# Optimization experiments

Measured on AMD Instinct MI355X. Metric: run time of the kernel, lower is better.

Reference implementation:

```python
import jax, jax.numpy as jnp
import numpy as np

N_EMBD = 384
N_HEADS = 6
HEAD_SIZE = N_EMBD // N_HEADS  # 64
D_FF = 4 * N_EMBD
EPS = 1e-5


def layernorm(x, g, b):
    mu = jnp.mean(x, axis=-1, keepdims=True)
    var = jnp.var(x, axis=-1, keepdims=True)
    return (x - mu) * jax.lax.rsqrt(var + EPS) * g + b


def setup_inputs() -> dict:
    key = jax.random.key(0)
    ks = jax.random.split(key, 12)
    B, T, C, H, HS = 64, 256, N_EMBD, N_HEADS, HEAD_SIZE
    s = 0.02
    return {
        "x": jax.random.normal(ks[0], (B, T, C), jnp.float32),
        "Wq": jax.random.normal(ks[1], (H, C, HS), jnp.float32) * s,
        "Wk": jax.random.normal(ks[2], (H, C, HS), jnp.float32) * s,
        "Wv": jax.random.normal(ks[3], (H, C, HS), jnp.float32) * s,
        "Wo": jax.random.normal(ks[4], (C, C), jnp.float32) * s,
        "bo": jnp.zeros((C,), jnp.float32),
        "W1": jax.random.normal(ks[5], (C, D_FF), jnp.float32) * s,
        "b1": jnp.zeros((D_FF,), jnp.float32),
        "W2": jax.random.normal(ks[6], (D_FF, C), jnp.float32) * s,
        "b2": jnp.zeros((C,), jnp.float32),
        "g1": jnp.ones((C,), jnp.float32),
        "beta1": jnp.zeros((C,), jnp.float32),
        "g2": jnp.ones((C,), jnp.float32),
        "beta2": jnp.zeros((C,), jnp.float32),
    }


def reference(x, Wq, Wk, Wv, Wo, bo, W1, b1, W2, b2, g1, beta1, g2, beta2):
    B, T, C = x.shape
    # --- attention branch (dropout = identity in eval) ---
    h = layernorm(x, g1, beta1)
    q = jnp.einsum('btc,hck->bhtk', h, Wq)
    k = jnp.einsum('btc,hck->bhtk', h, Wk)
    v = jnp.einsum('btc,hck->bhtk', h, Wv)
    scale = HEAD_SIZE ** -0.5
    wei = jnp.einsum('bhtk,bhsk->bhts', q, k) * scale  # [B,H,T,T]
    causal = jnp.tril(jnp.ones((T, T), bool))
    wei = jnp.where(causal, wei, -jnp.inf)
    wei = jax.nn.softmax(wei, axis=-1)
    attn = jnp.einsum('bhts,bhsk->bthk', wei, v).reshape(B, T, C)
    x = x + attn @ Wo + bo
    # --- MLP branch ---
    h2 = layernorm(x, g2, beta2)
    ff = jax.nn.relu(h2 @ W1 + b1) @ W2 + b2
    return x + ff
```

## Files before the change

### kernel.cpp

```cpp
#include <hip/hip_runtime.h>

#define B 64
#define T 256
#define C 384
#define H 6
#define HS 64
#define DFF 1536
#define BT (B*T)

typedef __attribute__((ext_vector_type(8))) short short8;
typedef __attribute__((ext_vector_type(4))) float float4v;
typedef __attribute__((ext_vector_type(4))) unsigned short ushort4v;

static __device__ __forceinline__ unsigned short f2bf(float f) {
  unsigned int u = __float_as_uint(f);
  unsigned int r = (u + 0x7fffu + ((u >> 16) & 1u)) >> 16;
  return (unsigned short)r;
}

typedef __attribute__((address_space(1))) const unsigned int ga_u32;
typedef __attribute__((address_space(3))) unsigned int ls_u32;
static __device__ __forceinline__ void gld16(const void* g, void* l) {
  __builtin_amdgcn_global_load_lds((ga_u32*)g, (ls_u32*)l, 16, 0, 0);
}

__global__ __launch_bounds__(256) void prep_w(
    const float* __restrict__ Wq, const float* __restrict__ Wk, const float* __restrict__ Wv,
    const float* __restrict__ Wo, const float* __restrict__ W1, const float* __restrict__ W2,
    unsigned short* __restrict__ wqkv, unsigned short* __restrict__ wo,
    unsigned short* __restrict__ w1t, unsigned short* __restrict__ w2t) {
  __shared__ float tile[32][33];
  int bx = blockIdx.x;
  int x = threadIdx.x & 31, y = threadIdx.x >> 5;
  if (bx < 432) {
    int tn = bx % 36, tc = bx / 36;
    int n0 = tn * 32, c0 = tc * 32;
    int mat = n0 / 384, rem = n0 % 384, head = rem / 64, hs0 = rem % 64;
    const float* W = (mat == 0) ? Wq : ((mat == 1) ? Wk : Wv);
    const float* src = W + (size_t)head * C * HS + hs0;
    #pragma unroll
    for (int i = 0; i < 4; ++i) tile[y + 8 * i][x] = src[(size_t)(c0 + y + 8 * i) * 64 + x];
    __syncthreads();
    #pragma unroll
    for (int i = 0; i < 4; ++i)
      wqkv[(size_t)(n0 + y + 8 * i) * 384 + c0 + x] = f2bf(tile[x][y + 8 * i]);
    return;
  }
  const float* src; unsigned short* dst; int CN, R, n0, c0;
  if (bx < 576) {
    int t = bx - 432; n0 = (t % 12) * 32; c0 = (t / 12) * 32;
    src = Wo; dst = wo; CN = 384; R = 384;
  } else if (bx < 1152) {
    int t = bx - 576; n0 = (t % 48) * 32; c0 = (t / 48) * 32;
    src = W1; dst = w1t; CN = 1536; R = 384;
  } else {
    int t = bx - 1152; n0 = (t % 12) * 32; c0 = (t / 12) * 32;
    src = W2; dst = w2t; CN = 384; R = 1536;
  }
  #pragma unroll
  for (int i = 0; i < 4; ++i) tile[y + 8 * i][x] = src[(size_t)(c0 + y + 8 * i) * CN + n0 + x];
  __syncthreads();
  #pragma unroll
  for (int i = 0; i < 4; ++i)
    dst[(size_t)(n0 + y + 8 * i) * R + c0 + x] = f2bf(tile[x][y + 8 * i]);
}

__global__ __launch_bounds__(64) void ln_kernel(const float* __restrict__ x,
    const float* __restrict__ g, const float* __restrict__ bta,
    unsigned short* __restrict__ out) {
  int t = blockIdx.x;
  int lane = threadIdx.x;
  const float* row = x + (size_t)t * C;
  float v[6];
  float s = 0.f, ss = 0.f;
  #pragma unroll
  for (int i = 0; i < 6; ++i) {
    v[i] = row[lane + i * 64];
    s += v[i];
    ss += v[i] * v[i];
  }
  #pragma unroll
  for (int m = 32; m >= 1; m >>= 1) {
    s += __shfl_xor(s, m);
    ss += __shfl_xor(ss, m);
  }
  float mu = s / C;
  float var = ss / C - mu * mu;
  float rstd = rsqrtf(var + 1e-5f);
  unsigned short* orow = out + (size_t)t * C;
  #pragma unroll
  for (int i = 0; i < 6; ++i) {
    int c = lane + i * 64;
    orow[c] = f2bf((v[i] - mu) * rstd * g[c] + bta[c]);
  }
}

template<int EPI, int MT>
__global__ __launch_bounds__(256) void gemm_kernel(
    const unsigned short* __restrict__ A, const unsigned short* __restrict__ Wt,
    const float* __restrict__ bias, const float* __restrict__ resid,
    float* __restrict__ outf,
    unsigned short* __restrict__ outb, unsigned short* __restrict__ outb2,
    unsigned short* __restrict__ outb3, int K, int N) {
  __shared__ unsigned short Ash[MT * 64];
  __shared__ unsigned short Bsh[128 * 64];
  constexpr int MR = MT / 32;
  constexpr int NA = MT / 32;
  int tid = threadIdx.x, lane = tid & 63, w = tid >> 6;
  int wm = w >> 1, wn = w & 1;
  int m0 = blockIdx.x * MT, n0 = blockIdx.y * 128;
  int lrow = lane >> 3;
  int lchunk = (lane & 7) ^ (lrow & 7);
  int frow = lane & 15, cg = lane >> 4;
  float4v acc[MR][4] = {};
  for (int k0 = 0; k0 < K; k0 += 64) {
    __syncthreads();
    #pragma unroll
    for (int i = 0; i < NA; ++i)
      gld16(A + (size_t)(m0 + w * (NA * 8) + i * 8 + lrow) * K + k0 + lchunk * 8,
            &Ash[(w * NA + i) * 512]);
    #pragma unroll
    for (int i = 0; i < 4; ++i)
      gld16(Wt + (size_t)(n0 + w * 32 + i * 8 + lrow) * K + k0 + lchunk * 8,
            &Bsh[(w * 4 + i) * 512]);
    __syncthreads();
    #pragma unroll
    for (int ks = 0; ks < 2; ++ks) {
      short8 af[MR], bf[4];
      #pragma unroll
      for (int mi = 0; mi < MR; ++mi) {
        int r = wm * (MR * 16) + mi * 16 + frow;
        int ch = (ks * 4 + cg) ^ (r & 7);
        af[mi] = *(const short8*)((const char*)Ash + r * 128 + ch * 16);
      }
      #pragma unroll
      for (int ni = 0; ni < 4; ++ni) {
        int r = wn * 64 + ni * 16 + frow;
        int ch = (ks * 4 + cg) ^ (r & 7);
        bf[ni] = *(const short8*)((const char*)Bsh + r * 128 + ch * 16);
      }
      #pragma unroll
      for (int mi = 0; mi < MR; ++mi)
        #pragma unroll
        for (int ni = 0; ni < 4; ++ni)
          acc[mi][ni] = __builtin_amdgcn_mfma_f32_16x16x32_bf16(af[mi], bf[ni], acc[mi][ni], 0, 0, 0);
    }
  }
  int cl = lane & 15;
  #pragma unroll
  for (int mi = 0; mi < MR; ++mi) {
    #pragma unroll
    for (int ni = 0; ni < 4; ++ni) {
      if constexpr (EPI == 0) {
        int gc = n0 + wn * 64 + ni * 16 + cl;
        int mat = gc / 384;
        int head = (gc % 384) >> 6;
        int hs = gc & 63;
        int gr0 = m0 + wm * (MR * 16) + mi * 16 + cg * 4;
        int tt0 = gr0 & 255, bidx = gr0 >> 8;
        size_t bhb = (size_t)(bidx * H + head);
        if (mat == 2) {
          ushort4v pk;
          #pragma unroll
          for (int j = 0; j < 4; ++j) pk[j] = f2bf(acc[mi][ni][j]);
          *(ushort4v*)&outb3[(bhb * HS + hs) * T + tt0] = pk;
        } else {
          unsigned short* dst = (mat == 0) ? outb : outb2;
          #pragma unroll
          for (int j = 0; j < 4; ++j)
            dst[(bhb * T + tt0 + j) * HS + hs] = f2bf(acc[mi][ni][j]);
        }
      } else {
        #pragma unroll
        for (int j = 0; j < 4; ++j) {
          int gr = m0 + wm * (MR * 16) + mi * 16 + cg * 4 + j;
          int gc = n0 + wn * 64 + ni * 16 + cl;
          float val = acc[mi][ni][j];
          if constexpr (EPI == 1) {
            size_t i = (size_t)gr * N + gc;
            outf[i] = resid[i] + val + bias[gc];
          } else if constexpr (EPI == 2) {
            outb[(size_t)gr * N + gc] = f2bf(fmaxf(val + bias[gc], 0.f));
          } else {
            size_t i = (size_t)gr * N + gc;
            outf[i] = resid[i] + val + bias[gc];
          }
        }
      }
    }
  }
}

__global__ __launch_bounds__(256) void attn_kernel(
    const unsigned short* __restrict__ qg, const unsigned short* __restrict__ kg,
    const unsigned short* __restrict__ vtg, unsigned short* __restrict__ ab) {
  __shared__ unsigned short Ksh[64 * 64];
  __shared__ unsigned short Vsh[64 * 256];
  __shared__ unsigned short Psh[4 * 16 * 256];
  int bh = blockIdx.x;
  int bb = bh / H, hh = bh % H;
  int qt = blockIdx.y, q0 = qt * 64;
  int tid = threadIdx.x, lane = tid & 63, w = tid >> 6;
  int cl = lane & 15, cg = lane >> 4;
  const float scale_log2e = 0.125f * 1.44269504f;
  const unsigned short* qp = qg + ((size_t)bh * T) * HS;
  const unsigned short* kp = kg + ((size_t)bh * T) * HS;
  const unsigned short* vp = vtg + ((size_t)bh * HS) * T;

  short8 aq[2];
  #pragma unroll
  for (int k0 = 0; k0 < 2; ++k0)
    aq[k0] = *(const short8*)&qp[(size_t)(q0 + w * 16 + cl) * HS + cg * 8 + k0 * 32];

  #pragma unroll
  for (int i = 0; i < 8; ++i) {
    int idx = tid + i * 256;
    int r = idx >> 5, c16 = idx & 31;
    uint4 val = *(const uint4*)&vp[(size_t)r * T + c16 * 8];
    int byte = (r * 512 + c16 * 16) ^ ((r & 7) << 4);
    *(uint4*)((char*)Vsh + byte) = val;
  }

  float4v sacc[4][4] = {};
  for (int si = 0; si <= qt; ++si) {
    __syncthreads();
    #pragma unroll
    for (int i = 0; i < 2; ++i) {
      int idx = tid + i * 256;
      int r = idx >> 3, c16 = idx & 7;
      uint4 val = *(const uint4*)&kp[(size_t)(si * 64 + r) * HS + c16 * 8];
      int byte = (r * 128 + c16 * 16) ^ ((r & 7) << 4);
      *(uint4*)((char*)Ksh + byte) = val;
    }
    __syncthreads();
    #pragma unroll
    for (int ss = 0; ss < 4; ++ss) {
      if (ss == si) {
        #pragma unroll
        for (int nt = 0; nt < 4; ++nt) {
          int srow = nt * 16 + cl;
          #pragma unroll
          for (int k0 = 0; k0 < 2; ++k0) {
            int byte = (srow * 128 + (cg * 8 + k0 * 32) * 2) ^ ((srow & 7) << 4);
            short8 bf = *(const short8*)((char*)Ksh + byte);
            sacc[ss][nt] = __builtin_amdgcn_mfma_f32_16x16x32_bf16(aq[k0], bf, sacc[ss][nt], 0, 0, 0);
          }
        }
      }
    }
  }

  #pragma unroll
  for (int si = 0; si < 4; ++si) {
    if (si == qt) {
      #pragma unroll
      for (int nt = 0; nt < 4; ++nt) {
        int s = q0 + nt * 16 + cl;
        #pragma unroll
        for (int j = 0; j < 4; ++j) {
          int q = q0 + w * 16 + cg * 4 + j;
          if (s > q) sacc[si][nt][j] = -1e30f;
        }
      }
    }
  }

  float lj[4];
  #pragma unroll
  for (int j = 0; j < 4; ++j) {
    float m = -1e30f;
    #pragma unroll
    for (int si = 0; si < 4; ++si) if (si <= qt)
      #pragma unroll
      for (int nt = 0; nt < 4; ++nt) m = fmaxf(m, sacc[si][nt][j]);
    #pragma unroll
    for (int off = 1; off < 16; off <<= 1) m = fmaxf(m, __shfl_xor(m, off));
    float l = 0.f;
    #pragma unroll
    for (int si = 0; si < 4; ++si) if (si <= qt)
      #pragma unroll
      for (int nt = 0; nt < 4; ++nt) {
        float p0 = exp2f((sacc[si][nt][j] - m) * scale_log2e);
        sacc[si][nt][j] = p0;
        l += p0;
      }
    #pragma unroll
    for (int off = 1; off < 16; off <<= 1) l += __shfl_xor(l, off);
    lj[j] = 1.f / l;
  }

  char* pbase = (char*)Psh + w * 8192;
  #pragma unroll
  for (int si = 0; si < 4; ++si) if (si <= qt)
    #pragma unroll
    for (int nt = 0; nt < 4; ++nt)
      #pragma unroll
      for (int j = 0; j < 4; ++j) {
        int prow = cg * 4 + j, col = si * 64 + nt * 16 + cl;
        int byte = (prow * 512 + col * 2) ^ ((prow & 7) << 4);
        *(unsigned short*)(pbase + byte) = f2bf(sacc[si][nt][j]);
      }

  int nks = 2 * (qt + 1);
  #pragma unroll
  for (int nt = 0; nt < 4; ++nt) {
    float4v oacc = {};
    for (int ks = 0; ks < nks; ++ks) {
      int k = ks * 32 + cg * 8;
      int pbyte = (cl * 512 + k * 2) ^ ((cl & 7) << 4);
      short8 af = *(const short8*)(pbase + pbyte);
      int vr = nt * 16 + cl;
      int vbyte = (vr * 512 + k * 2) ^ ((vr & 7) << 4);
      short8 bf = *(const short8*)((char*)Vsh + vbyte);
      oacc = __builtin_amdgcn_mfma_f32_16x16x32_bf16(af, bf, oacc, 0, 0, 0);
    }
    #pragma unroll
    for (int j = 0; j < 4; ++j) {
      int t = q0 + w * 16 + cg * 4 + j;
      ab[((size_t)(bb * T + t)) * C + hh * 64 + nt * 16 + cl] = f2bf(oacc[j] * lj[j]);
    }
  }
}

extern "C" void kernel_launch(void* const* d_in, const int* in_sizes, int n_in,
                              void* d_out, int out_size, void* d_ws, size_t ws_size,
                              hipStream_t stream) {
  const float* x   = (const float*)d_in[0];
  const float* Wq  = (const float*)d_in[1];
  const float* Wk  = (const float*)d_in[2];
  const float* Wv  = (const float*)d_in[3];
  const float* Wo  = (const float*)d_in[4];
  const float* bo  = (const float*)d_in[5];
  const float* W1  = (const float*)d_in[6];
  const float* b1  = (const float*)d_in[7];
  const float* W2  = (const float*)d_in[8];
  const float* b2  = (const float*)d_in[9];
  const float* g1  = (const float*)d_in[10];
  const float* be1 = (const float*)d_in[11];
  const float* g2  = (const float*)d_in[12];
  const float* be2 = (const float*)d_in[13];
  float* out = (float*)d_out;
  float* ws = (float*)d_ws;

  unsigned short* wqkv_t = (unsigned short*)ws;
  unsigned short* wo_t   = wqkv_t + 442368;
  unsigned short* w1t    = wo_t + 147456;
  unsigned short* w2t    = w1t + 589824;
  float* base2 = ws + 884736;
  unsigned short* h  = (unsigned short*)base2;
  float* x2 = base2 + 3145728;
  unsigned short* ab = (unsigned short*)(x2 + 6291456);
  unsigned short* qb = (unsigned short*)(x2 + 6291456 + 3145728);
  unsigned short* kb = qb + 6291456;
  unsigned short* vt = kb + 6291456;
  unsigned short* ffb = ab;

  prep_w<<<1728, 256, 0, stream>>>(Wq, Wk, Wv, Wo, W1, W2, wqkv_t, wo_t, w1t, w2t);
  ln_kernel<<<BT, 64, 0, stream>>>(x, g1, be1, h);
  gemm_kernel<0, 128><<<dim3(128, 9), 256, 0, stream>>>(h, wqkv_t, nullptr, nullptr,
                                                        nullptr, qb, kb, vt, 384, 1152);
  attn_kernel<<<dim3(B * H, T / 64), 256, 0, stream>>>(qb, kb, vt, ab);
  gemm_kernel<1, 64><<<dim3(256, 3), 256, 0, stream>>>(ab, wo_t, bo, x,
                                                       x2, nullptr, nullptr, nullptr, 384, 384);
  ln_kernel<<<BT, 64, 0, stream>>>(x2, g2, be2, h);
  gemm_kernel<2, 128><<<dim3(128, 12), 256, 0, stream>>>(h, w1t, b1, nullptr,
                                                         nullptr, ffb, nullptr, nullptr, 384, 1536);
  gemm_kernel<3, 64><<<dim3(256, 3), 256, 0, stream>>>(ffb, w2t, b2, x2,
                                                       out, nullptr, nullptr, nullptr, 1536, 384);
}
```

Measured before the change: 153.9 us.

## Double-buffer GEMM LDS tiles with fragment-native layout and K-step 32

Rewrites the GEMM main loop to use two LDS buffers with a K-step of 32, issuing global-to-LDS loads for the next tile while MFMAs run on the current one. This leaves one barrier per iteration instead of two. The LDS layout is changed so each 16-row block is stored in MFMA fragment order, so fragments are read as contiguous lane*16 loads with no XOR swizzle. The trade-off is twice as many loop iterations, each with less MFMA work, and no explicit wait on the asynchronous LDS loads before the barrier.

```diff
diff --git a/kernel.cpp b/kernel.cpp
--- a/kernel.cpp
+++ b/kernel.cpp
@@ -102,51 +102,55 @@
     float* __restrict__ outf,
     unsigned short* __restrict__ outb, unsigned short* __restrict__ outb2,
     unsigned short* __restrict__ outb3, int K, int N) {
-  __shared__ unsigned short Ash[MT * 64];
-  __shared__ unsigned short Bsh[128 * 64];
+  __shared__ unsigned short Ash[2][MT * 32];
+  __shared__ unsigned short Bsh[2][128 * 32];
   constexpr int MR = MT / 32;
-  constexpr int NA = MT / 32;
+  constexpr int NA = MT / 64;
   int tid = threadIdx.x, lane = tid & 63, w = tid >> 6;
   int wm = w >> 1, wn = w & 1;
   int m0 = blockIdx.x * MT, n0 = blockIdx.y * 128;
-  int lrow = lane >> 3;
-  int lchunk = (lane & 7) ^ (lrow & 7);
-  int frow = lane & 15, cg = lane >> 4;
+  int fr = lane & 15, ch = lane >> 4;
   float4v acc[MR][4] = {};
-  for (int k0 = 0; k0 < K; k0 += 64) {
+  int nt = K / 32;
+
+  auto STAGE = [&](int b, int t) {
+    int k0 = t * 32;
+    #pragma unroll
+    for (int i = 0; i < NA; ++i) {
+      int win = w * NA + i;
+      gld16(A + (size_t)(m0 + win * 16 + fr) * K + k0 + ch * 8, &Ash[b][win * 512]);
+    }
+    #pragma unroll
+    for (int i = 0; i < 2; ++i) {
+      int win = w * 2 + i;
+      gld16(Wt + (size_t)(n0 + win * 16 + fr) * K + k0 + ch * 8, &Bsh[b][win * 512]);
+    }
+  };
+
+  STAGE(0, 0);
+  __syncthreads();
+  int buf = 0;
+  for (int t = 0; t < nt; ++t) {
+    if (t + 1 < nt) STAGE(buf ^ 1, t + 1);
+    const unsigned short* Ab = Ash[buf];
+    const unsigned short* Bb = Bsh[buf];
+    short8 af[MR], bf[4];
+    #pragma unroll
+    for (int mi = 0; mi < MR; ++mi)
+      af[mi] = *(const short8*)((const char*)Ab + (wm * MR + mi) * 1024 + lane * 16);
+    #pragma unroll
+    for (int ni = 0; ni < 4; ++ni)
+      bf[ni] = *(const short8*)((const char*)Bb + (wn * 4 + ni) * 1024 + lane * 16);
+    #pragma unroll
+    for (int mi = 0; mi < MR; ++mi)
+      #pragma unroll
+      for (int ni = 0; ni < 4; ++ni)
+        acc[mi][ni] = __builtin_amdgcn_mfma_f32_16x16x32_bf16(af[mi], bf[ni], acc[mi][ni], 0, 0, 0);
     __syncthreads();
-    #pragma unroll
-    for (int i = 0; i < NA; ++i)
-      gld16(A + (size_t)(m0 + w * (NA * 8) + i * 8 + lrow) * K + k0 + lchunk * 8,
-            &Ash[(w * NA + i) * 512]);
-    #pragma unroll
-    for (int i = 0; i < 4; ++i)
-      gld16(Wt + (size_t)(n0 + w * 32 + i * 8 + lrow) * K + k0 + lchunk * 8,
-            &Bsh[(w * 4 + i) * 512]);
-    __syncthreads();
-    #pragma unroll
-    for (int ks = 0; ks < 2; ++ks) {
-      short8 af[MR], bf[4];
-      #pragma unroll
-      for (int mi = 0; mi < MR; ++mi) {
-        int r = wm * (MR * 16) + mi * 16 + frow;
-        int ch = (ks * 4 + cg) ^ (r & 7);
-        af[mi] = *(const short8*)((const char*)Ash + r * 128 + ch * 16);
-      }
-      #pragma unroll
-      for (int ni = 0; ni < 4; ++ni) {
-        int r = wn * 64 + ni * 16 + frow;
-        int ch = (ks * 4 + cg) ^ (r & 7);
-        bf[ni] = *(const short8*)((const char*)Bsh + r * 128 + ch * 16);
-      }
-      #pragma unroll
-      for (int mi = 0; mi < MR; ++mi)
-        #pragma unroll
-        for (int ni = 0; ni < 4; ++ni)
-          acc[mi][ni] = __builtin_amdgcn_mfma_f32_16x16x32_bf16(af[mi], bf[ni], acc[mi][ni], 0, 0, 0);
-    }
-  }
-  int cl = lane & 15;
+    buf ^= 1;
+  }
+
+  int cl = lane & 15, cg = lane >> 4;
   #pragma unroll
   for (int mi = 0; mi < MR; ++mi) {
     #pragma unroll
```

After: 208.1 us. +35.2%, slower.
